# Performance work log

Measured on AMD Instinct MI355X. Metric: run time of the kernel, lower is better.

Reference implementation:

```python
import jax, jax.numpy as jnp
import numpy as np

DURATION = 100.0   # init kwarg: duration
RESOLUTION = 0.1   # init kwarg: resolution
OUT_LEN = int(DURATION / RESOLUTION) + 1  # 1001


def setup_inputs() -> dict:
    key = jax.random.key(0)
    k1, k2 = jax.random.split(key)
    B, S, D = 32, 4096, 256
    embed_batch = jax.random.normal(k1, (B, S, D), dtype=jnp.float32)
    # sorted timestamps spanning [0, DURATION]
    ts_batch = jnp.sort(jax.random.uniform(k2, (B, S), dtype=jnp.float32) * DURATION, axis=-1)
    return {"embed_batch": embed_batch, "ts_batch": ts_batch}


def reference(embed_batch, ts_batch):
    # embed_batch: [B, S, D], ts_batch: [B, S] (sorted along last dim)
    B, S, D = embed_batch.shape
    ts_new = jnp.linspace(0.0, DURATION, OUT_LEN).astype(embed_batch.dtype)  # [L]
    # batched searchsorted replaces the per-sample/per-channel Python loops
    idx = jax.vmap(lambda t: jnp.searchsorted(t, ts_new))(ts_batch)  # [B, L]
    idx = jnp.clip(idx, 1, S - 1)
    lo = idx - 1  # [B, L]
    hi = idx
    x_lo = jnp.take_along_axis(ts_batch, lo, axis=1)  # [B, L]
    x_hi = jnp.take_along_axis(ts_batch, hi, axis=1)
    y_lo = jnp.take_along_axis(embed_batch, lo[:, :, None], axis=1)  # [B, L, D]
    y_hi = jnp.take_along_axis(embed_batch, hi[:, :, None], axis=1)
    slope = (y_hi - y_lo) / (x_hi - x_lo)[:, :, None]
    y_new = slope * (ts_new[None, :, None] - x_lo[:, :, None]) + y_lo
    return y_new  # [B, OUT_LEN, D]
```

## Files before the change

### kernel.cpp

```cpp
#include <hip/hip_runtime.h>


#define RS_B 32
#define RS_S 4096
#define RS_D 256
#define RS_OUTLEN 1001

__global__ __launch_bounds__(64) void resample_kernel(
    const float* __restrict__ embed,
    const float* __restrict__ ts,
    float* __restrict__ out)
{
    const int bid = blockIdx.x;
    const int b = bid / RS_OUTLEN;
    const int l = bid - b * RS_OUTLEN;

    const float t = (float)((double)l * (100.0 / 1000.0));

    const float* __restrict__ tsr = ts + (size_t)b * RS_S;

    int lo = 0, hi = RS_S;
    while (lo < hi) {
        int mid = (lo + hi) >> 1;
        float v = tsr[mid];
        if (v < t) lo = mid + 1; else hi = mid;
    }
    int idx = lo;
    if (idx < 1) idx = 1;
    if (idx > RS_S - 1) idx = RS_S - 1;

    const float x_lo = tsr[idx - 1];
    const float x_hi = tsr[idx];
    const float inv_dx = 1.0f / (x_hi - x_lo);
    const float dt = t - x_lo;

    const int d4 = threadIdx.x;
    const float4* __restrict__ ylo =
        (const float4*)(embed + ((size_t)b * RS_S + (size_t)(idx - 1)) * RS_D) + d4;
    const float4* __restrict__ yhi =
        (const float4*)(embed + ((size_t)b * RS_S + (size_t)idx) * RS_D) + d4;

    float4 a = *ylo;
    float4 c = *yhi;
    float4 r;
    r.x = (c.x - a.x) * inv_dx * dt + a.x;
    r.y = (c.y - a.y) * inv_dx * dt + a.y;
    r.z = (c.z - a.z) * inv_dx * dt + a.z;
    r.w = (c.w - a.w) * inv_dx * dt + a.w;

    float4* __restrict__ op =
        (float4*)(out + ((size_t)b * RS_OUTLEN + (size_t)l) * RS_D) + d4;
    *op = r;
}

extern "C" void kernel_launch(void* const* d_in, const int* in_sizes, int n_in,
                              void* d_out, int out_size, void* d_ws, size_t ws_size,
                              hipStream_t stream) {
    const float* embed = (const float*)d_in[0];
    const float* ts    = (const float*)d_in[1];
    float* out         = (float*)d_out;

    const int nblocks = RS_B * RS_OUTLEN;
    resample_kernel<<<nblocks, 64, 0, stream>>>(embed, ts, out);
}
```

Before: 24.28 us.

## Replace serial binary search with two-level wave ballot search and pack four outputs per block

The 12-step serial binary search, where each step is a dependent global load, becomes a two-level wave-parallel search. In the first level each lane loads one chunk boundary, and a ballot plus popcount picks the chunk. In the second level each lane loads one element of that chunk, and a second ballot gives the exact index. Blocks now hold four waves, each computing a different output row, which cuts the block count fourfold. The search now has two dependent load rounds instead of about twelve, in exchange for more total ts loads per wave.

```diff
diff --git a/kernel.cpp b/kernel.cpp
--- a/kernel.cpp
+++ b/kernel.cpp
@@ -5,26 +5,31 @@
 #define RS_S 4096
 #define RS_D 256
 #define RS_OUTLEN 1001
+#define RS_LPB 4
 
-__global__ __launch_bounds__(64) void resample_kernel(
+__global__ __launch_bounds__(256) void resample_kernel(
     const float* __restrict__ embed,
     const float* __restrict__ ts,
     float* __restrict__ out)
 {
-    const int bid = blockIdx.x;
-    const int b = bid / RS_OUTLEN;
-    const int l = bid - b * RS_OUTLEN;
+    const int b = blockIdx.y;
+    const int wave = threadIdx.x >> 6;
+    const int lane = threadIdx.x & 63;
+    const int l = blockIdx.x * RS_LPB + wave;
+    if (l >= RS_OUTLEN) return;
 
     const float t = (float)((double)l * (100.0 / 1000.0));
 
     const float* __restrict__ tsr = ts + (size_t)b * RS_S;
 
-    int lo = 0, hi = RS_S;
-    while (lo < hi) {
-        int mid = (lo + hi) >> 1;
-        float v = tsr[mid];
-        if (v < t) lo = mid + 1; else hi = mid;
-    }
+    float s1 = tsr[lane * 64 + 63];
+    unsigned long long m1 = __ballot(s1 < t);
+    int c = __popcll(m1);
+    int chunk = c < 63 ? c : 63;
+    float s2 = tsr[chunk * 64 + lane];
+    unsigned long long m2 = __ballot(s2 < t);
+    int lo = chunk * 64 + __popcll(m2);
+
     int idx = lo;
     if (idx < 1) idx = 1;
     if (idx > RS_S - 1) idx = RS_S - 1;
@@ -34,22 +39,21 @@
     const float inv_dx = 1.0f / (x_hi - x_lo);
     const float dt = t - x_lo;
 
-    const int d4 = threadIdx.x;
     const float4* __restrict__ ylo =
-        (const float4*)(embed + ((size_t)b * RS_S + (size_t)(idx - 1)) * RS_D) + d4;
+        (const float4*)(embed + ((size_t)b * RS_S + (size_t)(idx - 1)) * RS_D) + lane;
     const float4* __restrict__ yhi =
-        (const float4*)(embed + ((size_t)b * RS_S + (size_t)idx) * RS_D) + d4;
+        (const float4*)(embed + ((size_t)b * RS_S + (size_t)idx) * RS_D) + lane;
 
     float4 a = *ylo;
-    float4 c = *yhi;
+    float4 cc = *yhi;
     float4 r;
-    r.x = (c.x - a.x) * inv_dx * dt + a.x;
-    r.y = (c.y - a.y) * inv_dx * dt + a.y;
-    r.z = (c.z - a.z) * inv_dx * dt + a.z;
-    r.w = (c.w - a.w) * inv_dx * dt + a.w;
+    r.x = (cc.x - a.x) * inv_dx * dt + a.x;
+    r.y = (cc.y - a.y) * inv_dx * dt + a.y;
+    r.z = (cc.z - a.z) * inv_dx * dt + a.z;
+    r.w = (cc.w - a.w) * inv_dx * dt + a.w;
 
     float4* __restrict__ op =
-        (float4*)(out + ((size_t)b * RS_OUTLEN + (size_t)l) * RS_D) + d4;
+        (float4*)(out + ((size_t)b * RS_OUTLEN + (size_t)l) * RS_D) + lane;
     *op = r;
 }
 
@@ -60,6 +64,6 @@
     const float* ts    = (const float*)d_in[1];
     float* out         = (float*)d_out;
 
-    const int nblocks = RS_B * RS_OUTLEN;
-    resample_kernel<<<nblocks, 64, 0, stream>>>(embed, ts, out);
+    dim3 grid((RS_OUTLEN + RS_LPB - 1) / RS_LPB, RS_B);
+    resample_kernel<<<grid, 256, 0, stream>>>(embed, ts, out);
 }
```

After: 22.43 us. 1.08x faster.

## Batch 16 output points per wavefront with lane-parallel searches and shuffles

Applied to the files above, without the earlier changes.

Each 64-thread block now handles 16 consecutive output timestamps. Lanes do the binary searches in parallel, with a fixed 12-step unrolled loop, and the index and weight are broadcast with shuffles before looping over the points to interpolate. The grid shrinks from about 32k tiny blocks to about 2k, which cuts launch and scheduling overhead and the serial search latency each block pays. The cost is less parallelism per block and a serial loop of 16 load-compute-store iterations per wave.

```diff
diff --git a/kernel.cpp b/kernel.cpp
--- a/kernel.cpp
+++ b/kernel.cpp
@@ -5,22 +5,27 @@
 #define RS_S 4096
 #define RS_D 256
 #define RS_OUTLEN 1001
+#define RS_PPW 16
 
 __global__ __launch_bounds__(64) void resample_kernel(
     const float* __restrict__ embed,
     const float* __restrict__ ts,
     float* __restrict__ out)
 {
-    const int bid = blockIdx.x;
-    const int b = bid / RS_OUTLEN;
-    const int l = bid - b * RS_OUTLEN;
+    const int b  = blockIdx.y;
+    const int l0 = blockIdx.x * RS_PPW;
+    const int lane = threadIdx.x;
+    const int p = lane & 15;
 
+    int l = l0 + p;
+    if (l > RS_OUTLEN - 1) l = RS_OUTLEN - 1;
     const float t = (float)((double)l * (100.0 / 1000.0));
 
     const float* __restrict__ tsr = ts + (size_t)b * RS_S;
 
     int lo = 0, hi = RS_S;
-    while (lo < hi) {
+#pragma unroll
+    for (int it = 0; it < 12; ++it) {
         int mid = (lo + hi) >> 1;
         float v = tsr[mid];
         if (v < t) lo = mid + 1; else hi = mid;
@@ -31,26 +36,30 @@
 
     const float x_lo = tsr[idx - 1];
     const float x_hi = tsr[idx];
-    const float inv_dx = 1.0f / (x_hi - x_lo);
-    const float dt = t - x_lo;
+    const float w1 = (t - x_lo) / (x_hi - x_lo);
 
-    const int d4 = threadIdx.x;
-    const float4* __restrict__ ylo =
-        (const float4*)(embed + ((size_t)b * RS_S + (size_t)(idx - 1)) * RS_D) + d4;
-    const float4* __restrict__ yhi =
-        (const float4*)(embed + ((size_t)b * RS_S + (size_t)idx) * RS_D) + d4;
+    const float4* __restrict__ ebase =
+        (const float4*)(embed + (size_t)b * RS_S * RS_D);
+    float4* __restrict__ obase =
+        (float4*)(out + ((size_t)b * RS_OUTLEN + (size_t)l0) * RS_D);
 
-    float4 a = *ylo;
-    float4 c = *yhi;
-    float4 r;
-    r.x = (c.x - a.x) * inv_dx * dt + a.x;
-    r.y = (c.y - a.y) * inv_dx * dt + a.y;
-    r.z = (c.z - a.z) * inv_dx * dt + a.z;
-    r.w = (c.w - a.w) * inv_dx * dt + a.w;
+#pragma unroll
+    for (int q = 0; q < RS_PPW; ++q) {
+        if (l0 + q > RS_OUTLEN - 1) break;
+        const int   sidx = __shfl(idx, q);
+        const float sw   = __shfl(w1,  q);
 
-    float4* __restrict__ op =
-        (float4*)(out + ((size_t)b * RS_OUTLEN + (size_t)l) * RS_D) + d4;
-    *op = r;
+        const float4* plo = ebase + (size_t)(sidx - 1) * (RS_D / 4) + lane;
+        const float4* phi = plo + (RS_D / 4);
+        float4 a = *plo;
+        float4 c = *phi;
+        float4 r;
+        r.x = a.x + (c.x - a.x) * sw;
+        r.y = a.y + (c.y - a.y) * sw;
+        r.z = a.z + (c.z - a.z) * sw;
+        r.w = a.w + (c.w - a.w) * sw;
+        *(obase + (size_t)q * (RS_D / 4) + lane) = r;
+    }
 }
 
 extern "C" void kernel_launch(void* const* d_in, const int* in_sizes, int n_in,
@@ -60,6 +69,6 @@
     const float* ts    = (const float*)d_in[1];
     float* out         = (float*)d_out;
 
-    const int nblocks = RS_B * RS_OUTLEN;
-    resample_kernel<<<nblocks, 64, 0, stream>>>(embed, ts, out);
+    dim3 grid((RS_OUTLEN + RS_PPW - 1) / RS_PPW, RS_B);
+    resample_kernel<<<grid, 64, 0, stream>>>(embed, ts, out);
 }
```

Result: faster. 22.05 us (-9.2%).
